# Performance work log

Measured on AMD Instinct MI355X. Metric: run time of the kernel, lower is better.

Reference implementation:

```python
import jax, jax.numpy as jnp
import numpy as np

N_QUBITS = 8
INPUT_DIM = 32
HIDDEN_DIM = 8  # must equal N_QUBITS (gate outputs multiply cell state elementwise)
BATCH = 1024
SEQ_LEN = 64


def _cnot_perm(n):
    """Composite basis-state permutation for CNOT chain (0,1)..(n-2,n-1) then ring (n-1,0).
    Wire 0 is the most-significant bit. Returns gather indices: new[k] = old[perm[k]]."""
    idx = np.arange(2 ** n)
    gates = [(w, w + 1) for w in range(n - 1)] + [(n - 1, 0)]
    for c, t in reversed(gates):  # compose g1(g2(...gm(k)))
        sc, st = n - 1 - c, n - 1 - t
        idx = idx ^ (((idx >> sc) & 1) << st)
    return jnp.asarray(idx)


def _z_signs(n):
    """signs[k, i] = +1 if bit i of basis state k is 0 else -1 (PauliZ eigenvalue)."""
    k = np.arange(2 ** n)[:, None]
    w = (n - 1 - np.arange(n))[None, :]
    return jnp.asarray((1 - 2 * ((k >> w) & 1)).astype(np.float32))


_PERM = _cnot_perm(N_QUBITS)
_SIGNS = _z_signs(N_QUBITS)


def _qlayer(y, theta):
    """Exact statevector sim of: RX(y_i) encoder + trainable RX(theta_i) per wire,
    CNOT chain + ring, MeasureAll(PauliZ).
    RX gates on |0> give a product state with real/imaginary amplitude split, and
    CNOTs are phase-free basis permutations, so PauliZ expectations depend only on
    basis probabilities: p0=cos^2(a/2), p1=sin^2(a/2) with a = y + theta."""
    a = 0.5 * (y + theta)                                    # (B, n)
    p = jnp.stack([jnp.cos(a) ** 2, jnp.sin(a) ** 2], -1)    # (B, n, 2)
    probs = p[:, 0]                                          # (B, 2)
    for w in range(1, p.shape[1]):                           # small fixed loop over wires
        probs = (probs[:, :, None] * p[:, w, None, :]).reshape(probs.shape[0], -1)
    probs = probs[:, _PERM]                                  # apply CNOT permutation
    return probs @ _SIGNS                                    # (B, n) <Z_i>


def setup_inputs() -> dict:
    key = jax.random.key(0)
    ks = jax.random.split(key, 13)
    d = INPUT_DIM + HIDDEN_DIM
    s = 1.0 / np.sqrt(d)
    inp = {"inputs": jax.random.normal(ks[0], (BATCH, SEQ_LEN, INPUT_DIM), jnp.float32)}
    for j, nm in enumerate(["forget", "input", "update", "output"]):
        inp[f"W_{nm}"] = jax.random.uniform(ks[1 + 3 * j], (N_QUBITS, d), jnp.float32, -s, s)
        inp[f"b_{nm}"] = jax.random.uniform(ks[2 + 3 * j], (N_QUBITS,), jnp.float32, -s, s)
        inp[f"theta_{nm}"] = jax.random.uniform(ks[3 + 3 * j], (N_QUBITS,), jnp.float32, -np.pi, np.pi)
    return inp


def reference(inputs, W_forget, b_forget, theta_forget,
              W_input, b_input, theta_input,
              W_update, b_update, theta_update,
              W_output, b_output, theta_output):
    B = inputs.shape[0]
    hx0 = jnp.zeros((B, HIDDEN_DIM), inputs.dtype)
    cx0 = jnp.zeros((B, HIDDEN_DIM), inputs.dtype)

    def step(carry, x):
        hx, cx = carry
        comb = jnp.concatenate([x, hx], axis=-1)
        f = jax.nn.sigmoid(_qlayer(comb @ W_forget.T + b_forget, theta_forget))
        i = jax.nn.sigmoid(_qlayer(comb @ W_input.T + b_input, theta_input))
        g = jnp.tanh(_qlayer(comb @ W_update.T + b_update, theta_update))
        o = jax.nn.sigmoid(_qlayer(comb @ W_output.T + b_output, theta_output))
        cx2 = f * cx + i * g
        hx2 = o * jnp.tanh(cx2)
        return (hx2, cx2), hx2

    (hx, cx), ys = jax.lax.scan(step, (hx0, cx0), jnp.swapaxes(inputs, 0, 1))
    out_seq = jnp.swapaxes(ys, 0, 1)  # (B, T, hidden)
    return out_seq, hx, cx
```

## Files before the change

### kernel.cpp

```cpp
#include <hip/hip_runtime.h>

#define B_TOT 1024
#define SEQ 64
#define IND 32
#define HID 8

template<int CTRL>
__device__ __forceinline__ float dppf(float v) {
    return __int_as_float(__builtin_amdgcn_update_dpp(
        0, __float_as_int(v), CTRL, 0xF, 0xF, true));
}
template<int OFF>
__device__ __forceinline__ float swzf(float v) {
    return __int_as_float(__builtin_amdgcn_ds_swizzle(__float_as_int(v), OFF));
}

__global__ __launch_bounds__(64, 1) void qlstm_kernel(
    const float* __restrict__ xin,
    const float* __restrict__ Wf, const float* __restrict__ bf, const float* __restrict__ thf,
    const float* __restrict__ Wi, const float* __restrict__ bi, const float* __restrict__ thi,
    const float* __restrict__ Wu, const float* __restrict__ bu, const float* __restrict__ thu,
    const float* __restrict__ Wo, const float* __restrict__ bo, const float* __restrict__ tho,
    float* __restrict__ out)
{
    const int lane = threadIdx.x & 63;
    const int l32  = lane & 31;
    const int gate = l32 >> 3;
    const int row  = l32 & 7;
    const int b    = blockIdx.x * 2 + (lane >> 5);

    const float* Wg = (gate == 0) ? Wf : (gate == 1) ? Wi : (gate == 2) ? Wu : Wo;
    const float* bg = (gate == 0) ? bf : (gate == 1) ? bi : (gate == 2) ? bu : bo;
    const float* tg = (gate == 0) ? thf : (gate == 1) ? thi : (gate == 2) ? thu : tho;

    float4 wx[8];
    const float4* wp = (const float4*)(Wg + row * 40);
    #pragma unroll
    for (int k = 0; k < 8; ++k) wx[k] = wp[k];
    float wh[8];
    #pragma unroll
    for (int k = 0; k < 8; ++k) wh[k] = Wg[row * 40 + 32 + k];
    const float bt = bg[row] + tg[row];

    const float es = (gate == 2) ? 2.0f : -1.0f;
    const float aA = (gate == 2) ? 1.0f : 0.0f;
    const float aB = (gate == 2) ? -2.0f : 1.0f;

    const float* xbase = xin + (size_t)b * (SEQ * IND);
    float* oseq = out + (size_t)b * (SEQ * HID);

    float hxv[8] = {0,0,0,0,0,0,0,0};
    float cx = 0.0f, hlast = 0.0f;

    float4 xa[8], xb[8];
    {
        const float4* p = (const float4*)xbase;
        #pragma unroll
        for (int k = 0; k < 8; ++k) xa[k] = p[k];
    }

    auto loadx = [&](float4 (&xv)[8], int t) {
        const float4* p = (const float4*)(xbase + t * IND);
        #pragma unroll
        for (int k = 0; k < 8; ++k) xv[k] = p[k];
    };

    auto step = [&](const float4 (&xv)[8], int t) {
        float d0 = bt, d1 = 0.f, d2 = 0.f, d3 = 0.f;
        #pragma unroll
        for (int k = 0; k < 8; ++k) {
            d0 = fmaf(wx[k].x, xv[k].x, d0);
            d1 = fmaf(wx[k].y, xv[k].y, d1);
            d2 = fmaf(wx[k].z, xv[k].z, d2);
            d3 = fmaf(wx[k].w, xv[k].w, d3);
        }
        d0 = fmaf(wh[0], hxv[0], d0); d1 = fmaf(wh[1], hxv[1], d1);
        d2 = fmaf(wh[2], hxv[2], d2); d3 = fmaf(wh[3], hxv[3], d3);
        d0 = fmaf(wh[4], hxv[4], d0); d1 = fmaf(wh[5], hxv[5], d1);
        d2 = fmaf(wh[6], hxv[6], d2); d3 = fmaf(wh[7], hxv[7], d3);
        float y = (d0 + d1) + (d2 + d3);

        float r = y * 0.15915494309189535f;
        r = __builtin_amdgcn_fractf(r);
        float c = __builtin_amdgcn_cosf(r);

        float v = c;
        float w = (row == 0) ? 1.0f : c;
        float tv, tw;
        tv = dppf<0x111>(v); tw = dppf<0x111>(w);
        if (row >= 1) { v *= tv; w *= tw; }
        tv = dppf<0x112>(v); tw = dppf<0x112>(w);
        if (row >= 2) { v *= tv; w *= tw; }
        tv = dppf<0x114>(v); tw = dppf<0x114>(w);
        if (row >= 4) { v *= tv; w *= tw; }
        float full = dppf<0x141>(w);
        float q = (row == 0) ? full : v;

        float e  = __expf(q * es);
        float rr = __builtin_amdgcn_rcpf(1.0f + e);
        float act = fmaf(aB, rr, aA);

        float iv = swzf<0x201f>(act);
        float gv = swzf<0x401f>(act);
        float ov = swzf<0x601f>(act);

        cx = fmaf(act, cx, iv * gv);
        float e2 = __expf(2.0f * cx);
        float th = 1.0f - 2.0f * __builtin_amdgcn_rcpf(1.0f + e2);
        float h2 = ov * th;
        hlast = h2;

        if (l32 < 8) oseq[t * HID + row] = h2;

        hxv[0] = swzf<0x000>(h2);
        hxv[1] = swzf<0x020>(h2);
        hxv[2] = swzf<0x040>(h2);
        hxv[3] = swzf<0x060>(h2);
        hxv[4] = swzf<0x080>(h2);
        hxv[5] = swzf<0x0A0>(h2);
        hxv[6] = swzf<0x0C0>(h2);
        hxv[7] = swzf<0x0E0>(h2);
    };

    #pragma unroll 1
    for (int t = 0; t < SEQ; t += 2) {
        loadx(xb, t + 1);
        step(xa, t);
        loadx(xa, (t + 2) & 63);
        step(xb, t + 1);
    }

    if (l32 < 8) {
        out[(size_t)B_TOT * SEQ * HID + b * HID + row] = hlast;
        out[(size_t)B_TOT * SEQ * HID + B_TOT * HID + b * HID + row] = cx;
    }
}

extern "C" void kernel_launch(void* const* d_in, const int* in_sizes, int n_in,
                              void* d_out, int out_size, void* d_ws, size_t ws_size,
                              hipStream_t stream) {
    qlstm_kernel<<<512, 64, 0, stream>>>(
        (const float*)d_in[0],
        (const float*)d_in[1],  (const float*)d_in[2],  (const float*)d_in[3],
        (const float*)d_in[4],  (const float*)d_in[5],  (const float*)d_in[6],
        (const float*)d_in[7],  (const float*)d_in[8],  (const float*)d_in[9],
        (const float*)d_in[10], (const float*)d_in[11], (const float*)d_in[12],
        (float*)d_out);
}
```

Before: 30.06 us.

## Precompute input projections in parallel into LDS, run recurrence with DPP-only exchanges

The x·W input projection for all timesteps is computed in parallel by 512 threads per block and stored in shared memory before the sequential recurrence. A single wave then runs the recurrence for 4 batch rows, each lane handling two gates and exchanging hidden state and gate values through DPP instead of ds_swizzle. The aim is to take the 32-wide dot product and the global x loads off the serial critical path and to shorten the per-step cross-lane latency. In exchange, 448 of the 512 threads sit idle during the recurrence and the grid shrinks to 256 blocks.

```diff
diff --git a/kernel.cpp b/kernel.cpp
--- a/kernel.cpp
+++ b/kernel.cpp
@@ -4,18 +4,15 @@
 #define SEQ 64
 #define IND 32
 #define HID 8
+#define BPB 4
 
 template<int CTRL>
 __device__ __forceinline__ float dppf(float v) {
     return __int_as_float(__builtin_amdgcn_update_dpp(
         0, __float_as_int(v), CTRL, 0xF, 0xF, true));
 }
-template<int OFF>
-__device__ __forceinline__ float swzf(float v) {
-    return __int_as_float(__builtin_amdgcn_ds_swizzle(__float_as_int(v), OFF));
-}
 
-__global__ __launch_bounds__(64, 1) void qlstm_kernel(
+__global__ __launch_bounds__(512, 1) void qlstm_kernel(
     const float* __restrict__ xin,
     const float* __restrict__ Wf, const float* __restrict__ bf, const float* __restrict__ thf,
     const float* __restrict__ Wi, const float* __restrict__ bi, const float* __restrict__ thi,
@@ -23,123 +20,149 @@
     const float* __restrict__ Wo, const float* __restrict__ bo, const float* __restrict__ tho,
     float* __restrict__ out)
 {
-    const int lane = threadIdx.x & 63;
-    const int l32  = lane & 31;
-    const int gate = l32 >> 3;
-    const int row  = l32 & 7;
-    const int b    = blockIdx.x * 2 + (lane >> 5);
+    __shared__ float zs[BPB][SEQ + 1][33];
 
-    const float* Wg = (gate == 0) ? Wf : (gate == 1) ? Wi : (gate == 2) ? Wu : Wo;
-    const float* bg = (gate == 0) ? bf : (gate == 1) ? bi : (gate == 2) ? bu : bo;
-    const float* tg = (gate == 0) ? thf : (gate == 1) ? thi : (gate == 2) ? thu : tho;
+    const int tid = threadIdx.x;
 
-    float4 wx[8];
-    const float4* wp = (const float4*)(Wg + row * 40);
-    #pragma unroll
-    for (int k = 0; k < 8; ++k) wx[k] = wp[k];
-    float wh[8];
-    #pragma unroll
-    for (int k = 0; k < 8; ++k) wh[k] = Wg[row * 40 + 32 + k];
-    const float bt = bg[row] + tg[row];
+    {
+        const int sub = tid >> 8;
+        const int idx = tid & 255;
+        const int bl  = idx >> 6;
+        const int t   = idx & 63;
+        const int gb  = blockIdx.x * BPB + bl;
+        const float4* xp = (const float4*)(xin + ((size_t)gb * SEQ + t) * IND);
+        float4 x4[8];
+        #pragma unroll
+        for (int k = 0; k < 8; ++k) x4[k] = xp[k];
 
-    const float es = (gate == 2) ? 2.0f : -1.0f;
-    const float aA = (gate == 2) ? 1.0f : 0.0f;
-    const float aB = (gate == 2) ? -2.0f : 1.0f;
-
-    const float* xbase = xin + (size_t)b * (SEQ * IND);
-    float* oseq = out + (size_t)b * (SEQ * HID);
-
-    float hxv[8] = {0,0,0,0,0,0,0,0};
-    float cx = 0.0f, hlast = 0.0f;
-
-    float4 xa[8], xb[8];
-    {
-        const float4* p = (const float4*)xbase;
         #pragma unroll
-        for (int k = 0; k < 8; ++k) xa[k] = p[k];
+        for (int j = 0; j < 16; ++j) {
+            const int row = j & 7;
+            const float* W = sub ? (j < 8 ? Wu : Wo) : (j < 8 ? Wf : Wi);
+            const float* B = sub ? (j < 8 ? bu : bo) : (j < 8 ? bf : bi);
+            const float* T = sub ? (j < 8 ? thu : tho) : (j < 8 ? thf : thi);
+            const float4* wr = (const float4*)(W + row * 40);
+            float a0 = B[row] + T[row], a1 = 0.f, a2 = 0.f, a3 = 0.f;
+            #pragma unroll
+            for (int k = 0; k < 8; ++k) {
+                float4 w4 = wr[k];
+                a0 = fmaf(w4.x, x4[k].x, a0);
+                a1 = fmaf(w4.y, x4[k].y, a1);
+                a2 = fmaf(w4.z, x4[k].z, a2);
+                a3 = fmaf(w4.w, x4[k].w, a3);
+            }
+            zs[bl][t][(sub << 4) | j] = (a0 + a1) + (a2 + a3);
+        }
     }
 
-    auto loadx = [&](float4 (&xv)[8], int t) {
-        const float4* p = (const float4*)(xbase + t * IND);
-        #pragma unroll
-        for (int k = 0; k < 8; ++k) xv[k] = p[k];
-    };
+    __syncthreads();
+    if (tid >= 64) return;
 
-    auto step = [&](const float4 (&xv)[8], int t) {
-        float d0 = bt, d1 = 0.f, d2 = 0.f, d3 = 0.f;
+    const int lane = tid;
+    const int b    = lane >> 4;
+    const int l16  = lane & 15;
+    const int p    = l16 >> 3;
+    const int r    = l16 & 7;
+    const int gb   = blockIdx.x * BPB + b;
+    const bool isP0 = (p == 0);
+
+    const int m[8] = {0, 1, 2, 3, 7, 6, 5, 4};
+    const float* WA = p ? Wi : Wf;
+    const float* WB = p ? Wo : Wu;
+    float whA[8], whB[8];
+    #pragma unroll
+    for (int k = 0; k < 8; ++k) {
+        whA[k] = WA[r * 40 + 32 + (r ^ m[k])];
+        whB[k] = WB[r * 40 + 32 + (r ^ m[k])];
+    }
+    const float esB = p ? -1.0f : 2.0f;
+    const float cAB = p ? 0.0f : 1.0f;
+    const float cBB = p ? 1.0f : -2.0f;
+
+    float* obase = out + (size_t)gb * (SEQ * HID);
+
+    float cx = 0.f, hlast = 0.f;
+    float hv[8] = {0.f, 0.f, 0.f, 0.f, 0.f, 0.f, 0.f, 0.f};
+    float zA = zs[b][0][p * 8 + r];
+    float zB = zs[b][0][p * 8 + r + 16];
+
+    #pragma unroll 2
+    for (int t = 0; t < SEQ; ++t) {
+        const int tn = (t + 1) & 63;
+        float zAn = zs[b][tn][p * 8 + r];
+        float zBn = zs[b][tn][p * 8 + r + 16];
+
+        float yA = zA, yB = zB;
         #pragma unroll
         for (int k = 0; k < 8; ++k) {
-            d0 = fmaf(wx[k].x, xv[k].x, d0);
-            d1 = fmaf(wx[k].y, xv[k].y, d1);
-            d2 = fmaf(wx[k].z, xv[k].z, d2);
-            d3 = fmaf(wx[k].w, xv[k].w, d3);
+            yA = fmaf(whA[k], hv[k], yA);
+            yB = fmaf(whB[k], hv[k], yB);
         }
-        d0 = fmaf(wh[0], hxv[0], d0); d1 = fmaf(wh[1], hxv[1], d1);
-        d2 = fmaf(wh[2], hxv[2], d2); d3 = fmaf(wh[3], hxv[3], d3);
-        d0 = fmaf(wh[4], hxv[4], d0); d1 = fmaf(wh[5], hxv[5], d1);
-        d2 = fmaf(wh[6], hxv[6], d2); d3 = fmaf(wh[7], hxv[7], d3);
-        float y = (d0 + d1) + (d2 + d3);
 
-        float r = y * 0.15915494309189535f;
-        r = __builtin_amdgcn_fractf(r);
-        float c = __builtin_amdgcn_cosf(r);
+        float cA = __builtin_amdgcn_cosf(__builtin_amdgcn_fractf(yA * 0.15915494309189535f));
+        float cB = __builtin_amdgcn_cosf(__builtin_amdgcn_fractf(yB * 0.15915494309189535f));
 
-        float v = c;
-        float w = (row == 0) ? 1.0f : c;
-        float tv, tw;
-        tv = dppf<0x111>(v); tw = dppf<0x111>(w);
-        if (row >= 1) { v *= tv; w *= tw; }
-        tv = dppf<0x112>(v); tw = dppf<0x112>(w);
-        if (row >= 2) { v *= tv; w *= tw; }
-        tv = dppf<0x114>(v); tw = dppf<0x114>(w);
-        if (row >= 4) { v *= tv; w *= tw; }
-        float full = dppf<0x141>(w);
-        float q = (row == 0) ? full : v;
+        float vA = cA, wA = (r == 0) ? 1.0f : cA;
+        float vB = cB, wB = (r == 0) ? 1.0f : cB;
+        float tA, uA, tB, uB;
+        tA = dppf<0x111>(vA); uA = dppf<0x111>(wA);
+        tB = dppf<0x111>(vB); uB = dppf<0x111>(wB);
+        vA *= (r >= 1) ? tA : 1.0f;  wA *= (r >= 1) ? uA : 1.0f;
+        vB *= (r >= 1) ? tB : 1.0f;  wB *= (r >= 1) ? uB : 1.0f;
+        tA = dppf<0x112>(vA); uA = dppf<0x112>(wA);
+        tB = dppf<0x112>(vB); uB = dppf<0x112>(wB);
+        vA *= (r >= 2) ? tA : 1.0f;  wA *= (r >= 2) ? uA : 1.0f;
+        vB *= (r >= 2) ? tB : 1.0f;  wB *= (r >= 2) ? uB : 1.0f;
+        tA = dppf<0x114>(vA); uA = dppf<0x114>(wA);
+        tB = dppf<0x114>(vB); uB = dppf<0x114>(wB);
+        vA *= (r >= 4) ? tA : 1.0f;  wA *= (r >= 4) ? uA : 1.0f;
+        vB *= (r >= 4) ? tB : 1.0f;  wB *= (r >= 4) ? uB : 1.0f;
+        float fmA = dppf<0x141>(wA);
+        float fmB = dppf<0x141>(wB);
+        float qA = (r == 0) ? fmA : vA;
+        float qB = (r == 0) ? fmB : vB;
 
-        float e  = __expf(q * es);
-        float rr = __builtin_amdgcn_rcpf(1.0f + e);
-        float act = fmaf(aB, rr, aA);
+        float actA = __builtin_amdgcn_rcpf(1.0f + __expf(-qA));
+        float actB = fmaf(cBB, __builtin_amdgcn_rcpf(1.0f + __expf(qB * esB)), cAB);
 
-        float iv = swzf<0x201f>(act);
-        float gv = swzf<0x401f>(act);
-        float ov = swzf<0x601f>(act);
+        float oA = dppf<0x128>(actA);
+        float oB = dppf<0x128>(actB);
+        float fv = isP0 ? actA : oA;
+        float iv = isP0 ? oA : actA;
+        float gv = isP0 ? actB : oB;
+        float ov = isP0 ? oB : actB;
 
-        cx = fmaf(act, cx, iv * gv);
+        cx = fmaf(fv, cx, iv * gv);
         float e2 = __expf(2.0f * cx);
         float th = 1.0f - 2.0f * __builtin_amdgcn_rcpf(1.0f + e2);
-        float h2 = ov * th;
-        hlast = h2;
+        float h  = ov * th;
+        hlast = h;
 
-        if (l32 < 8) oseq[t * HID + row] = h2;
+        if (isP0) obase[t * HID + r] = h;
 
-        hxv[0] = swzf<0x000>(h2);
-        hxv[1] = swzf<0x020>(h2);
-        hxv[2] = swzf<0x040>(h2);
-        hxv[3] = swzf<0x060>(h2);
-        hxv[4] = swzf<0x080>(h2);
-        hxv[5] = swzf<0x0A0>(h2);
-        hxv[6] = swzf<0x0C0>(h2);
-        hxv[7] = swzf<0x0E0>(h2);
-    };
+        hv[0] = h;
+        hv[1] = dppf<0xB1>(h);
+        hv[2] = dppf<0x4E>(hv[0]);
+        hv[3] = dppf<0x4E>(hv[1]);
+        hv[4] = dppf<0x141>(hv[0]);
+        hv[5] = dppf<0x141>(hv[1]);
+        hv[6] = dppf<0x141>(hv[2]);
+        hv[7] = dppf<0x141>(hv[3]);
 
-    #pragma unroll 1
-    for (int t = 0; t < SEQ; t += 2) {
-        loadx(xb, t + 1);
-        step(xa, t);
-        loadx(xa, (t + 2) & 63);
-        step(xb, t + 1);
+        zA = zAn; zB = zBn;
     }
 
-    if (l32 < 8) {
-        out[(size_t)B_TOT * SEQ * HID + b * HID + row] = hlast;
-        out[(size_t)B_TOT * SEQ * HID + B_TOT * HID + b * HID + row] = cx;
+    if (isP0) {
+        const size_t hx_off = (size_t)B_TOT * SEQ * HID;
+        out[hx_off + (size_t)gb * HID + r] = hlast;
+        out[hx_off + (size_t)B_TOT * HID + (size_t)gb * HID + r] = cx;
     }
 }
 
 extern "C" void kernel_launch(void* const* d_in, const int* in_sizes, int n_in,
                               void* d_out, int out_size, void* d_ws, size_t ws_size,
                               hipStream_t stream) {
-    qlstm_kernel<<<512, 64, 0, stream>>>(
+    qlstm_kernel<<<256, 512, 0, stream>>>(
         (const float*)d_in[0],
         (const float*)d_in[1],  (const float*)d_in[2],  (const float*)d_in[3],
         (const float*)d_in[4],  (const float*)d_in[5],  (const float*)d_in[6],
```

Result: no change. 30.04 us (-0.1%).
